# Kernel optimization log

Measured on AMD Instinct MI355X. Metric: run time of the kernel, lower is better.

Reference implementation:

```python
import jax, jax.numpy as jnp
import numpy as np

D = 128        # node_representation_size
V = 100000     # unique_internal_nodes (embedding vocab)
N = 20000      # nodes in the internal graph
E = 640000     # total neighbor (edge) entries


def setup_inputs() -> dict:
    key = jax.random.key(0)
    k1, k2, k3, k4, k5, k6 = jax.random.split(key, 6)
    node_ids = jax.random.randint(k1, (N,), 0, V)
    neighbor_ids = jax.random.randint(k2, (E,), 0, V)
    segment_ids = jnp.sort(jax.random.randint(k3, (E,), 0, N))
    xav = 1.0 / np.sqrt(D)  # xavier_normal std for square [D,D]
    W = jax.random.normal(k4, (D, D), dtype=jnp.float32) * xav
    M = jax.random.normal(k5, (D, D), dtype=jnp.float32) * xav
    emb = jax.random.normal(k6, (V, D), dtype=jnp.float32)
    return {"node_ids": node_ids, "neighbor_ids": neighbor_ids,
            "segment_ids": segment_ids, "W": W, "M": M, "emb": emb}


def reference(node_ids, neighbor_ids, segment_ids, W, M, emb):
    # Per node: s = relu(W @ e[node] + sum_{nbr} M @ e[nbr]); result = sum_nodes s
    self_term = emb[node_ids] @ W.T                       # [N, D]
    nb_msgs = emb[neighbor_ids] @ M.T                     # [E, D]
    nb_agg = jax.ops.segment_sum(nb_msgs, segment_ids, num_segments=N)  # [N, D]
    per_node = jax.nn.relu(self_term + nb_agg)            # [N, D]
    result = per_node.sum(axis=0)                         # [D]
    return jax.nn.softmax(result)[:, None]                # [D, 1], softmax over dim 0
```

## Files before the change

### kernel.cpp

```cpp
#include <hip/hip_runtime.h>

#define D 128
#define RS_STRIDE 64
#define MV_BLOCKS 1024

typedef __attribute__((ext_vector_type(8))) short bf16x8;
typedef __attribute__((ext_vector_type(4))) float f32x4;

__device__ __forceinline__ unsigned short f2bf(float f) {
    unsigned u = __float_as_uint(f);
    unsigned r = (u + 0x7fffu + ((u >> 16) & 1u)) >> 16;
    return (unsigned short)r;
}
__device__ __forceinline__ ushort4 pack4(float4 v) {
    ushort4 o; o.x = f2bf(v.x); o.y = f2bf(v.y); o.z = f2bf(v.z); o.w = f2bf(v.w);
    return o;
}
__device__ __forceinline__ void red3(float& x) {
    x += __shfl_xor(x, 8);
    x += __shfl_xor(x, 16);
    x += __shfl_xor(x, 32);
}

__global__ void rowptr_kernel(const int* __restrict__ seg, int* __restrict__ row_ptr,
                              float* __restrict__ rs, int E, int N) {
    int e = blockIdx.x * blockDim.x + threadIdx.x;
    if (e < D) rs[e * RS_STRIDE] = 0.0f;
    if (e >= E) return;
    int s = seg[e];
    if (e == 0) {
        for (int n = 0; n <= s; ++n) row_ptr[n] = 0;
    } else {
        int sp = seg[e - 1];
        for (int n = sp + 1; n <= s; ++n) row_ptr[n] = e;
    }
    if (e == E - 1) {
        for (int n = s + 1; n <= N; ++n) row_ptr[n] = E;
    }
}

__global__ void prep_kernel(const float* __restrict__ W, const float* __restrict__ M,
                            unsigned short* __restrict__ Wb, unsigned short* __restrict__ Mb) {
    int i = blockIdx.x * blockDim.x + threadIdx.x;
    if (i < D * D) { Wb[i] = f2bf(W[i]); Mb[i] = f2bf(M[i]); }
}

__global__ void agg_kernel(const int* __restrict__ node_ids, const int* __restrict__ nbr,
                           const int* __restrict__ row_ptr, const float* __restrict__ emb,
                           unsigned short* __restrict__ aggb, unsigned short* __restrict__ xb,
                           int N) {
    int n = blockIdx.x * 4 + (threadIdx.x >> 6);
    if (n >= N) return;
    int tt = threadIdx.x & 63;
    int c = tt & 7;
    int j = tt >> 3;

    int lo = row_ptr[n];
    int hi = row_ptr[n + 1];

    float4 s0 = make_float4(0.f, 0.f, 0.f, 0.f);
    float4 s1 = make_float4(0.f, 0.f, 0.f, 0.f);
    float4 s2 = make_float4(0.f, 0.f, 0.f, 0.f);
    float4 s3 = make_float4(0.f, 0.f, 0.f, 0.f);

    for (int e = lo + j; e < hi; e += 8) {
        const float4* r = (const float4*)&emb[(size_t)nbr[e] * D];
        float4 v0 = r[c], v1 = r[c + 8], v2 = r[c + 16], v3 = r[c + 24];
        s0.x += v0.x; s0.y += v0.y; s0.z += v0.z; s0.w += v0.w;
        s1.x += v1.x; s1.y += v1.y; s1.z += v1.z; s1.w += v1.w;
        s2.x += v2.x; s2.y += v2.y; s2.z += v2.z; s2.w += v2.w;
        s3.x += v3.x; s3.y += v3.y; s3.z += v3.z; s3.w += v3.w;
    }
    red3(s0.x); red3(s0.y); red3(s0.z); red3(s0.w);
    red3(s1.x); red3(s1.y); red3(s1.z); red3(s1.w);
    red3(s2.x); red3(s2.y); red3(s2.z); red3(s2.w);
    red3(s3.x); red3(s3.y); red3(s3.z); red3(s3.w);

    if (j == 0) {
        ushort4* o = (ushort4*)(aggb + (size_t)n * D);
        o[c]      = pack4(s0);
        o[c + 8]  = pack4(s1);
        o[c + 16] = pack4(s2);
        o[c + 24] = pack4(s3);
    }
    if (tt < 32) {
        int nid = node_ids[n];
        float4 v = ((const float4*)&emb[(size_t)nid * D])[tt];
        ((ushort4*)(xb + (size_t)n * D))[tt] = pack4(v);
    }
}

__global__ __launch_bounds__(256) void matvec_kernel(
    const unsigned short* __restrict__ xb, const unsigned short* __restrict__ aggb,
    const unsigned short* __restrict__ Wb, const unsigned short* __restrict__ Mb,
    float* __restrict__ rs, int N, int ngroups) {
    int t = threadIdx.x;
    int wid = blockIdx.x * 4 + (t >> 6);
    int l = t & 63;
    int quad = l >> 4, col = l & 15;
    int dt = wid & 7;
    int stripe = wid >> 3;

    bf16x8 bw[4], bm[4];
    int wrow = (dt * 16 + col) * D;
#pragma unroll
    for (int ks = 0; ks < 4; ++ks) {
        int off = wrow + ks * 32 + quad * 8;
        bw[ks] = *(const bf16x8*)(Wb + off);
        bm[ks] = *(const bf16x8*)(Mb + off);
    }

    const bf16x8 zero8 = {0, 0, 0, 0, 0, 0, 0, 0};
    float vsum = 0.f;

    for (int grp = stripe; grp < ngroups; grp += 512) {
        int node = grp * 16 + col;
        bool valid = node < N;
        const unsigned short* xr = xb + (size_t)node * D + quad * 8;
        const unsigned short* ar = aggb + (size_t)node * D + quad * 8;

        f32x4 acc = {0.f, 0.f, 0.f, 0.f};
#pragma unroll
        for (int ks = 0; ks < 4; ++ks) {
            bf16x8 ax = valid ? *(const bf16x8*)(xr + ks * 32) : zero8;
            bf16x8 aa = valid ? *(const bf16x8*)(ar + ks * 32) : zero8;
            acc = __builtin_amdgcn_mfma_f32_16x16x32_bf16(ax, bw[ks], acc, 0, 0, 0);
            acc = __builtin_amdgcn_mfma_f32_16x16x32_bf16(aa, bm[ks], acc, 0, 0, 0);
        }
        vsum += fmaxf(acc[0], 0.f) + fmaxf(acc[1], 0.f)
              + fmaxf(acc[2], 0.f) + fmaxf(acc[3], 0.f);
    }

    vsum += __shfl_xor(vsum, 16);
    vsum += __shfl_xor(vsum, 32);
    if (l < 16) atomicAdd(&rs[(dt * 16 + col) * RS_STRIDE], vsum);
}

__global__ void softmax_kernel(const float* __restrict__ rs, float* __restrict__ out) {
    int t = threadIdx.x;
    float v0 = rs[t * RS_STRIDE];
    float v1 = rs[(t + 64) * RS_STRIDE];
    float m = fmaxf(v0, v1);
    for (int o = 32; o > 0; o >>= 1) m = fmaxf(m, __shfl_xor(m, o));
    float e0 = expf(v0 - m);
    float e1 = expf(v1 - m);
    float s = e0 + e1;
    for (int o = 32; o > 0; o >>= 1) s += __shfl_xor(s, o);
    float inv = 1.0f / s;
    out[t] = e0 * inv;
    out[t + 64] = e1 * inv;
}

extern "C" void kernel_launch(void* const* d_in, const int* in_sizes, int n_in,
                              void* d_out, int out_size, void* d_ws, size_t ws_size,
                              hipStream_t stream) {
    const int*   node_ids = (const int*)d_in[0];
    const int*   nbr      = (const int*)d_in[1];
    const int*   seg      = (const int*)d_in[2];
    const float* W        = (const float*)d_in[3];
    const float* M        = (const float*)d_in[4];
    const float* emb      = (const float*)d_in[5];
    float* out = (float*)d_out;

    int N = in_sizes[0];
    int E = in_sizes[1];
    int ngroups = (N + 15) / 16;

    unsigned short* xb   = (unsigned short*)d_ws;
    unsigned short* aggb = xb + (size_t)N * D;
    unsigned short* Wb   = aggb + (size_t)N * D;
    unsigned short* Mb   = Wb + D * D;
    float* rs            = (float*)(Mb + D * D);
    int* row_ptr         = (int*)(rs + D * RS_STRIDE);

    rowptr_kernel<<<(E + 255) / 256, 256, 0, stream>>>(seg, row_ptr, rs, E, N);
    prep_kernel<<<(D * D + 255) / 256, 256, 0, stream>>>(W, M, Wb, Mb);
    agg_kernel<<<(N + 3) / 4, 256, 0, stream>>>(node_ids, nbr, row_ptr, emb, aggb, xb, N);
    matvec_kernel<<<MV_BLOCKS, 256, 0, stream>>>(xb, aggb, Wb, Mb, rs, N, ngroups);
    softmax_kernel<<<1, 64, 0, stream>>>(rs, out);
}
```

Before: 155.8 us.

## Convert embedding table to bf16 per call and gather bf16 rows

A new conversion kernel turns the whole fp32 embedding table, plus W and M, into bf16 in the workspace on every call. The neighbor aggregation then gathers half-width rows. The self-node gather moves into the MFMA matvec kernel, which reads bf16 rows by node id, so the separate xb buffer goes away. The matvec grid now scales with the group count instead of a fixed block count. In exchange, every call pays a full-table read and write, and neighbor sums are built from bf16-rounded inputs, with an fp32 fallback when the workspace is too small.

```diff
diff --git a/kernel.cpp b/kernel.cpp
--- a/kernel.cpp
+++ b/kernel.cpp
@@ -2,9 +2,9 @@
 
 #define D 128
 #define RS_STRIDE 64
-#define MV_BLOCKS 1024
 
 typedef __attribute__((ext_vector_type(8))) short bf16x8;
+typedef __attribute__((ext_vector_type(8))) unsigned short u16x8;
 typedef __attribute__((ext_vector_type(4))) float f32x4;
 
 __device__ __forceinline__ unsigned short f2bf(float f) {
@@ -12,6 +12,9 @@
     unsigned r = (u + 0x7fffu + ((u >> 16) & 1u)) >> 16;
     return (unsigned short)r;
 }
+__device__ __forceinline__ float bf2f(unsigned short h) {
+    return __uint_as_float(((unsigned)h) << 16);
+}
 __device__ __forceinline__ ushort4 pack4(float4 v) {
     ushort4 o; o.x = f2bf(v.x); o.y = f2bf(v.y); o.z = f2bf(v.z); o.w = f2bf(v.w);
     return o;
@@ -22,10 +25,20 @@
     x += __shfl_xor(x, 32);
 }
 
+__global__ void convert_kernel(const float* __restrict__ emb, const float* __restrict__ W,
+                               const float* __restrict__ M, unsigned short* __restrict__ embb,
+                               unsigned short* __restrict__ Wb, unsigned short* __restrict__ Mb,
+                               float* __restrict__ rs, int n4) {
+    int i = blockIdx.x * blockDim.x + threadIdx.x;
+    if (i < n4) ((ushort4*)embb)[i] = pack4(((const float4*)emb)[i]);
+    if (i < 4096)       ((ushort4*)Wb)[i]        = pack4(((const float4*)W)[i]);
+    else if (i < 8192)  ((ushort4*)Mb)[i - 4096] = pack4(((const float4*)M)[i - 4096]);
+    if (i < D) rs[i * RS_STRIDE] = 0.0f;
+}
+
 __global__ void rowptr_kernel(const int* __restrict__ seg, int* __restrict__ row_ptr,
-                              float* __restrict__ rs, int E, int N) {
+                              int E, int N) {
     int e = blockIdx.x * blockDim.x + threadIdx.x;
-    if (e < D) rs[e * RS_STRIDE] = 0.0f;
     if (e >= E) return;
     int s = seg[e];
     if (e == 0) {
@@ -39,30 +52,56 @@
     }
 }
 
-__global__ void prep_kernel(const float* __restrict__ W, const float* __restrict__ M,
-                            unsigned short* __restrict__ Wb, unsigned short* __restrict__ Mb) {
-    int i = blockIdx.x * blockDim.x + threadIdx.x;
-    if (i < D * D) { Wb[i] = f2bf(W[i]); Mb[i] = f2bf(M[i]); }
-}
-
-__global__ void agg_kernel(const int* __restrict__ node_ids, const int* __restrict__ nbr,
-                           const int* __restrict__ row_ptr, const float* __restrict__ emb,
-                           unsigned short* __restrict__ aggb, unsigned short* __restrict__ xb,
-                           int N) {
+__global__ void agg_bf_kernel(const int* __restrict__ nbr, const int* __restrict__ row_ptr,
+                              const unsigned short* __restrict__ embb,
+                              unsigned short* __restrict__ aggb, int N) {
     int n = blockIdx.x * 4 + (threadIdx.x >> 6);
     if (n >= N) return;
     int tt = threadIdx.x & 63;
     int c = tt & 7;
     int j = tt >> 3;
 
-    int lo = row_ptr[n];
-    int hi = row_ptr[n + 1];
+    int lo = row_ptr[n], hi = row_ptr[n + 1];
+
+    float s0[8], s1[8];
+#pragma unroll
+    for (int k = 0; k < 8; ++k) { s0[k] = 0.f; s1[k] = 0.f; }
+
+    for (int e = lo + j; e < hi; e += 8) {
+        const u16x8* r = (const u16x8*)(embb + (size_t)nbr[e] * D);
+        u16x8 v0 = r[c];
+        u16x8 v1 = r[c + 8];
+#pragma unroll
+        for (int k = 0; k < 8; ++k) { s0[k] += bf2f(v0[k]); s1[k] += bf2f(v1[k]); }
+    }
+#pragma unroll
+    for (int k = 0; k < 8; ++k) { red3(s0[k]); red3(s1[k]); }
+
+    if (j == 0) {
+        u16x8 o0, o1;
+#pragma unroll
+        for (int k = 0; k < 8; ++k) { o0[k] = f2bf(s0[k]); o1[k] = f2bf(s1[k]); }
+        u16x8* o = (u16x8*)(aggb + (size_t)n * D);
+        o[c] = o0;
+        o[c + 8] = o1;
+    }
+}
+
+__global__ void agg_f32_kernel(const int* __restrict__ nbr, const int* __restrict__ row_ptr,
+                               const float* __restrict__ emb,
+                               unsigned short* __restrict__ aggb, int N) {
+    int n = blockIdx.x * 4 + (threadIdx.x >> 6);
+    if (n >= N) return;
+    int tt = threadIdx.x & 63;
+    int c = tt & 7;
+    int j = tt >> 3;
+
+    int lo = row_ptr[n], hi = row_ptr[n + 1];
 
     float4 s0 = make_float4(0.f, 0.f, 0.f, 0.f);
     float4 s1 = make_float4(0.f, 0.f, 0.f, 0.f);
     float4 s2 = make_float4(0.f, 0.f, 0.f, 0.f);
     float4 s3 = make_float4(0.f, 0.f, 0.f, 0.f);
-
     for (int e = lo + j; e < hi; e += 8) {
         const float4* r = (const float4*)&emb[(size_t)nbr[e] * D];
         float4 v0 = r[c], v1 = r[c + 8], v2 = r[c + 16], v3 = r[c + 24];
@@ -75,7 +114,6 @@
     red3(s1.x); red3(s1.y); red3(s1.z); red3(s1.w);
     red3(s2.x); red3(s2.y); red3(s2.z); red3(s2.w);
     red3(s3.x); red3(s3.y); red3(s3.z); red3(s3.w);
-
     if (j == 0) {
         ushort4* o = (ushort4*)(aggb + (size_t)n * D);
         o[c]      = pack4(s0);
@@ -83,17 +121,14 @@
         o[c + 16] = pack4(s2);
         o[c + 24] = pack4(s3);
     }
-    if (tt < 32) {
-        int nid = node_ids[n];
-        float4 v = ((const float4*)&emb[(size_t)nid * D])[tt];
-        ((ushort4*)(xb + (size_t)n * D))[tt] = pack4(v);
-    }
-}
-
+}
+
+template <bool BF>
 __global__ __launch_bounds__(256) void matvec_kernel(
-    const unsigned short* __restrict__ xb, const unsigned short* __restrict__ aggb,
+    const int* __restrict__ node_ids, const void* __restrict__ embv,
+    const unsigned short* __restrict__ aggb,
     const unsigned short* __restrict__ Wb, const unsigned short* __restrict__ Mb,
-    float* __restrict__ rs, int N, int ngroups) {
+    float* __restrict__ rs, int N, int ngroups, int nstripes) {
     int t = threadIdx.x;
     int wid = blockIdx.x * 4 + (t >> 6);
     int l = t & 63;
@@ -113,16 +148,32 @@
     const bf16x8 zero8 = {0, 0, 0, 0, 0, 0, 0, 0};
     float vsum = 0.f;
 
-    for (int grp = stripe; grp < ngroups; grp += 512) {
+    for (int grp = stripe; grp < ngroups; grp += nstripes) {
         int node = grp * 16 + col;
         bool valid = node < N;
-        const unsigned short* xr = xb + (size_t)node * D + quad * 8;
+        int nid = valid ? node_ids[node] : 0;
         const unsigned short* ar = aggb + (size_t)node * D + quad * 8;
 
         f32x4 acc = {0.f, 0.f, 0.f, 0.f};
 #pragma unroll
         for (int ks = 0; ks < 4; ++ks) {
-            bf16x8 ax = valid ? *(const bf16x8*)(xr + ks * 32) : zero8;
+            bf16x8 ax;
+            if (BF) {
+                const unsigned short* xr =
+                    (const unsigned short*)embv + (size_t)nid * D + quad * 8;
+                ax = valid ? *(const bf16x8*)(xr + ks * 32) : zero8;
+            } else {
+                if (valid) {
+                    const float4* xf = (const float4*)((const float*)embv +
+                                       (size_t)nid * D + quad * 8 + ks * 32);
+                    ushort4 p0 = pack4(xf[0]);
+                    ushort4 p1 = pack4(xf[1]);
+                    ax[0] = (short)p0.x; ax[1] = (short)p0.y;
+                    ax[2] = (short)p0.z; ax[3] = (short)p0.w;
+                    ax[4] = (short)p1.x; ax[5] = (short)p1.y;
+                    ax[6] = (short)p1.z; ax[7] = (short)p1.w;
+                } else ax = zero8;
+            }
             bf16x8 aa = valid ? *(const bf16x8*)(ar + ks * 32) : zero8;
             acc = __builtin_amdgcn_mfma_f32_16x16x32_bf16(ax, bw[ks], acc, 0, 0, 0);
             acc = __builtin_amdgcn_mfma_f32_16x16x32_bf16(aa, bm[ks], acc, 0, 0, 0);
@@ -164,18 +215,33 @@
 
     int N = in_sizes[0];
     int E = in_sizes[1];
-    int ngroups = (N + 15) / 16;
-
-    unsigned short* xb   = (unsigned short*)d_ws;
-    unsigned short* aggb = xb + (size_t)N * D;
+    long long VD = in_sizes[5];
+    int ngroups  = (N + 15) / 16;
+    int nstripes = (ngroups + 1) / 2;
+    int mv_blocks = 2 * nstripes;
+
+    unsigned short* aggb = (unsigned short*)d_ws;
     unsigned short* Wb   = aggb + (size_t)N * D;
     unsigned short* Mb   = Wb + D * D;
     float* rs            = (float*)(Mb + D * D);
-    int* row_ptr         = (int*)(rs + D * RS_STRIDE);
-
-    rowptr_kernel<<<(E + 255) / 256, 256, 0, stream>>>(seg, row_ptr, rs, E, N);
-    prep_kernel<<<(D * D + 255) / 256, 256, 0, stream>>>(W, M, Wb, Mb);
-    agg_kernel<<<(N + 3) / 4, 256, 0, stream>>>(node_ids, nbr, row_ptr, emb, aggb, xb, N);
-    matvec_kernel<<<MV_BLOCKS, 256, 0, stream>>>(xb, aggb, Wb, Mb, rs, N, ngroups);
+    int* row_ptr         = (int*)(rs + (size_t)D * RS_STRIDE);
+    unsigned short* embb = (unsigned short*)(row_ptr + (N + 1));
+
+    size_t need_bf = (size_t)(row_ptr + (N + 1) - (int*)d_ws) * 4 + (size_t)VD * 2;
+    bool use_bf = ws_size >= need_bf;
+    int n4 = use_bf ? (int)(VD / 4) : 0;
+    int cvt_n = (n4 > 8192 ? n4 : 8192);
+
+    convert_kernel<<<(cvt_n + 255) / 256, 256, 0, stream>>>(emb, W, M, embb, Wb, Mb, rs, n4);
+    rowptr_kernel<<<(E + 255) / 256, 256, 0, stream>>>(seg, row_ptr, E, N);
+    if (use_bf) {
+        agg_bf_kernel<<<(N + 3) / 4, 256, 0, stream>>>(nbr, row_ptr, embb, aggb, N);
+        matvec_kernel<true><<<mv_blocks, 256, 0, stream>>>(node_ids, embb, aggb, Wb, Mb,
+                                                           rs, N, ngroups, nstripes);
+    } else {
+        agg_f32_kernel<<<(N + 3) / 4, 256, 0, stream>>>(nbr, row_ptr, emb, aggb, N);
+        matvec_kernel<false><<<mv_blocks, 256, 0, stream>>>(node_ids, emb, aggb, Wb, Mb,
+                                                            rs, N, ngroups, nstripes);
+    }
     softmax_kernel<<<1, 64, 0, stream>>>(rs, out);
 }
```

Result: no change. 153.1 us (-1.7%).

## Quantize embedding table to int8 per-row and gather quantized rows in aggregation

Applied to the files above, without the earlier changes.

Adds a prep pass that quantizes the whole embedding table to int8 with a per-row scale. Neighbor aggregation then gathers 128-byte int8 rows instead of 512-byte fp32 rows. The same pass merges row_ptr construction and the W/M bf16 conversion, removing separate launches. The self-term now reads fp32 embedding rows directly inside the matvec kernel instead of staging a bf16 copy, and the matvec grid is resized to the node count. The cost is a full read of the 51 MB table on every call to quantize it, plus int8 rounding error in the neighbor sums.

```diff
diff --git a/kernel.cpp b/kernel.cpp
--- a/kernel.cpp
+++ b/kernel.cpp
@@ -2,9 +2,10 @@
 
 #define D 128
 #define RS_STRIDE 64
-#define MV_BLOCKS 1024
 
 typedef __attribute__((ext_vector_type(8))) short bf16x8;
+typedef __attribute__((ext_vector_type(8))) unsigned short u16x8;
+typedef __attribute__((ext_vector_type(16))) char i8x16;
 typedef __attribute__((ext_vector_type(4))) float f32x4;
 
 __device__ __forceinline__ unsigned short f2bf(float f) {
@@ -16,84 +17,107 @@
     ushort4 o; o.x = f2bf(v.x); o.y = f2bf(v.y); o.z = f2bf(v.z); o.w = f2bf(v.w);
     return o;
 }
-__device__ __forceinline__ void red3(float& x) {
-    x += __shfl_xor(x, 8);
-    x += __shfl_xor(x, 16);
-    x += __shfl_xor(x, 32);
-}
-
-__global__ void rowptr_kernel(const int* __restrict__ seg, int* __restrict__ row_ptr,
-                              float* __restrict__ rs, int E, int N) {
-    int e = blockIdx.x * blockDim.x + threadIdx.x;
-    if (e < D) rs[e * RS_STRIDE] = 0.0f;
-    if (e >= E) return;
-    int s = seg[e];
-    if (e == 0) {
-        for (int n = 0; n <= s; ++n) row_ptr[n] = 0;
-    } else {
-        int sp = seg[e - 1];
-        for (int n = sp + 1; n <= s; ++n) row_ptr[n] = e;
-    }
-    if (e == E - 1) {
-        for (int n = s + 1; n <= N; ++n) row_ptr[n] = E;
-    }
-}
-
-__global__ void prep_kernel(const float* __restrict__ W, const float* __restrict__ M,
-                            unsigned short* __restrict__ Wb, unsigned short* __restrict__ Mb) {
-    int i = blockIdx.x * blockDim.x + threadIdx.x;
-    if (i < D * D) { Wb[i] = f2bf(W[i]); Mb[i] = f2bf(M[i]); }
-}
-
-__global__ void agg_kernel(const int* __restrict__ node_ids, const int* __restrict__ nbr,
-                           const int* __restrict__ row_ptr, const float* __restrict__ emb,
-                           unsigned short* __restrict__ aggb, unsigned short* __restrict__ xb,
-                           int N) {
+
+__global__ void prep_kernel(const float* __restrict__ emb, const float* __restrict__ W,
+                            const float* __restrict__ M, const int* __restrict__ seg,
+                            signed char* __restrict__ q8, float* __restrict__ scale,
+                            unsigned short* __restrict__ Wb, unsigned short* __restrict__ Mb,
+                            float* __restrict__ rs, int* __restrict__ row_ptr,
+                            int V, int E, int N) {
+    int t = threadIdx.x;
+    int gtid = blockIdx.x * 256 + t;
+
+    int r = blockIdx.x * 4 + (t >> 6);
+    if (r < V) {
+        int l = t & 63;
+        float2 v = *(const float2*)(emb + (size_t)r * D + 2 * l);
+        float m = fmaxf(fabsf(v.x), fabsf(v.y));
+        for (int o = 1; o < 64; o <<= 1) m = fmaxf(m, __shfl_xor(m, o));
+        float inv = (m > 0.f) ? 127.0f / m : 0.f;
+        int qa = __float2int_rn(v.x * inv);
+        int qb = __float2int_rn(v.y * inv);
+        qa = min(max(qa, -127), 127);
+        qb = min(max(qb, -127), 127);
+        unsigned short pq = (unsigned short)(((unsigned char)qb << 8) | (unsigned char)qa);
+        *(unsigned short*)(q8 + (size_t)r * D + 2 * l) = pq;
+        if (l == 0) scale[r] = m * (1.0f / 127.0f);
+    }
+
+    if (gtid < 4096)      ((ushort4*)Wb)[gtid]        = pack4(((const float4*)W)[gtid]);
+    else if (gtid < 8192) ((ushort4*)Mb)[gtid - 4096] = pack4(((const float4*)M)[gtid - 4096]);
+    if (gtid < D) rs[gtid * RS_STRIDE] = 0.0f;
+
+    if (gtid < E) {
+        int s = seg[gtid];
+        if (gtid == 0) {
+            for (int n = 0; n <= s; ++n) row_ptr[n] = 0;
+        } else {
+            int sp = seg[gtid - 1];
+            for (int n = sp + 1; n <= s; ++n) row_ptr[n] = gtid;
+        }
+        if (gtid == E - 1) {
+            for (int n = s + 1; n <= N; ++n) row_ptr[n] = E;
+        }
+    }
+}
+
+__global__ void agg_kernel(const int* __restrict__ nbr, const int* __restrict__ row_ptr,
+                           const signed char* __restrict__ q8, const float* __restrict__ scale,
+                           unsigned short* __restrict__ aggb, int N) {
     int n = blockIdx.x * 4 + (threadIdx.x >> 6);
     if (n >= N) return;
     int tt = threadIdx.x & 63;
-    int c = tt & 7;
-    int j = tt >> 3;
-
-    int lo = row_ptr[n];
-    int hi = row_ptr[n + 1];
-
-    float4 s0 = make_float4(0.f, 0.f, 0.f, 0.f);
-    float4 s1 = make_float4(0.f, 0.f, 0.f, 0.f);
-    float4 s2 = make_float4(0.f, 0.f, 0.f, 0.f);
-    float4 s3 = make_float4(0.f, 0.f, 0.f, 0.f);
-
-    for (int e = lo + j; e < hi; e += 8) {
-        const float4* r = (const float4*)&emb[(size_t)nbr[e] * D];
-        float4 v0 = r[c], v1 = r[c + 8], v2 = r[c + 16], v3 = r[c + 24];
-        s0.x += v0.x; s0.y += v0.y; s0.z += v0.z; s0.w += v0.w;
-        s1.x += v1.x; s1.y += v1.y; s1.z += v1.z; s1.w += v1.w;
-        s2.x += v2.x; s2.y += v2.y; s2.z += v2.z; s2.w += v2.w;
-        s3.x += v3.x; s3.y += v3.y; s3.z += v3.z; s3.w += v3.w;
-    }
-    red3(s0.x); red3(s0.y); red3(s0.z); red3(s0.w);
-    red3(s1.x); red3(s1.y); red3(s1.z); red3(s1.w);
-    red3(s2.x); red3(s2.y); red3(s2.z); red3(s2.w);
-    red3(s3.x); red3(s3.y); red3(s3.z); red3(s3.w);
+    int cc = tt & 3;
+    int j  = tt >> 2;
+
+    int lo = row_ptr[n], hi = row_ptr[n + 1];
+
+    float s[32];
+#pragma unroll
+    for (int k = 0; k < 32; ++k) s[k] = 0.f;
+
+    int e = lo + j;
+    int id = (e < hi) ? nbr[e] : -1;
+    while (id >= 0) {
+        const i8x16* r = (const i8x16*)(q8 + (size_t)id * D) + cc * 2;
+        float sc = scale[id];
+        int e2 = e + 16;
+        int id2 = (e2 < hi) ? nbr[e2] : -1;
+        i8x16 p0 = r[0], p1 = r[1];
+#pragma unroll
+        for (int k = 0; k < 16; ++k) {
+            s[k]      = fmaf((float)p0[k], sc, s[k]);
+            s[k + 16] = fmaf((float)p1[k], sc, s[k + 16]);
+        }
+        e = e2; id = id2;
+    }
+#pragma unroll
+    for (int k = 0; k < 32; ++k) {
+        float x = s[k];
+        x += __shfl_xor(x, 4);
+        x += __shfl_xor(x, 8);
+        x += __shfl_xor(x, 16);
+        x += __shfl_xor(x, 32);
+        s[k] = x;
+    }
 
     if (j == 0) {
-        ushort4* o = (ushort4*)(aggb + (size_t)n * D);
-        o[c]      = pack4(s0);
-        o[c + 8]  = pack4(s1);
-        o[c + 16] = pack4(s2);
-        o[c + 24] = pack4(s3);
-    }
-    if (tt < 32) {
-        int nid = node_ids[n];
-        float4 v = ((const float4*)&emb[(size_t)nid * D])[tt];
-        ((ushort4*)(xb + (size_t)n * D))[tt] = pack4(v);
+        u16x8* o = (u16x8*)(aggb + (size_t)n * D) + cc * 4;
+#pragma unroll
+        for (int q = 0; q < 4; ++q) {
+            u16x8 ov;
+#pragma unroll
+            for (int k = 0; k < 8; ++k) ov[k] = f2bf(s[q * 8 + k]);
+            o[q] = ov;
+        }
     }
 }
 
 __global__ __launch_bounds__(256) void matvec_kernel(
-    const unsigned short* __restrict__ xb, const unsigned short* __restrict__ aggb,
+    const int* __restrict__ node_ids, const float* __restrict__ emb,
+    const unsigned short* __restrict__ aggb,
     const unsigned short* __restrict__ Wb, const unsigned short* __restrict__ Mb,
-    float* __restrict__ rs, int N, int ngroups) {
+    float* __restrict__ rs, int N, int ngroups, int nstripes) {
     int t = threadIdx.x;
     int wid = blockIdx.x * 4 + (t >> 6);
     int l = t & 63;
@@ -113,16 +137,25 @@
     const bf16x8 zero8 = {0, 0, 0, 0, 0, 0, 0, 0};
     float vsum = 0.f;
 
-    for (int grp = stripe; grp < ngroups; grp += 512) {
+    for (int grp = stripe; grp < ngroups; grp += nstripes) {
         int node = grp * 16 + col;
         bool valid = node < N;
-        const unsigned short* xr = xb + (size_t)node * D + quad * 8;
+        int nid = valid ? node_ids[node] : 0;
         const unsigned short* ar = aggb + (size_t)node * D + quad * 8;
 
         f32x4 acc = {0.f, 0.f, 0.f, 0.f};
 #pragma unroll
         for (int ks = 0; ks < 4; ++ks) {
-            bf16x8 ax = valid ? *(const bf16x8*)(xr + ks * 32) : zero8;
+            bf16x8 ax;
+            if (valid) {
+                const float4* xf = (const float4*)(emb + (size_t)nid * D + quad * 8 + ks * 32);
+                ushort4 p0 = pack4(xf[0]);
+                ushort4 p1 = pack4(xf[1]);
+                ax[0] = (short)p0.x; ax[1] = (short)p0.y;
+                ax[2] = (short)p0.z; ax[3] = (short)p0.w;
+                ax[4] = (short)p1.x; ax[5] = (short)p1.y;
+                ax[6] = (short)p1.z; ax[7] = (short)p1.w;
+            } else ax = zero8;
             bf16x8 aa = valid ? *(const bf16x8*)(ar + ks * 32) : zero8;
             acc = __builtin_amdgcn_mfma_f32_16x16x32_bf16(ax, bw[ks], acc, 0, 0, 0);
             acc = __builtin_amdgcn_mfma_f32_16x16x32_bf16(aa, bm[ks], acc, 0, 0, 0);
@@ -164,18 +197,29 @@
 
     int N = in_sizes[0];
     int E = in_sizes[1];
-    int ngroups = (N + 15) / 16;
-
-    unsigned short* xb   = (unsigned short*)d_ws;
-    unsigned short* aggb = xb + (size_t)N * D;
-    unsigned short* Wb   = aggb + (size_t)N * D;
+    long long VD = in_sizes[5];
+    int V = (int)(VD / D);
+    int ngroups  = (N + 15) / 16;
+    int nstripes = (ngroups + 1) / 2;
+    int mv_blocks = 2 * nstripes;
+
+    signed char* q8      = (signed char*)d_ws;
+    float* scale         = (float*)(q8 + (size_t)V * D);
+    unsigned short* Wb   = (unsigned short*)(scale + V);
     unsigned short* Mb   = Wb + D * D;
-    float* rs            = (float*)(Mb + D * D);
-    int* row_ptr         = (int*)(rs + D * RS_STRIDE);
-
-    rowptr_kernel<<<(E + 255) / 256, 256, 0, stream>>>(seg, row_ptr, rs, E, N);
-    prep_kernel<<<(D * D + 255) / 256, 256, 0, stream>>>(W, M, Wb, Mb);
-    agg_kernel<<<(N + 3) / 4, 256, 0, stream>>>(node_ids, nbr, row_ptr, emb, aggb, xb, N);
-    matvec_kernel<<<MV_BLOCKS, 256, 0, stream>>>(xb, aggb, Wb, Mb, rs, N, ngroups);
+    unsigned short* aggb = Mb + D * D;
+    float* rs            = (float*)(aggb + (size_t)N * D);
+    int* row_ptr         = (int*)(rs + (size_t)D * RS_STRIDE);
+
+    int prep_blocks = (V + 3) / 4;
+    int min_blocks  = (E + 255) / 256;
+    if (prep_blocks < min_blocks) prep_blocks = min_blocks;
+    if (prep_blocks < 32) prep_blocks = 32;
+
+    prep_kernel<<<prep_blocks, 256, 0, stream>>>(emb, W, M, seg, q8, scale, Wb, Mb,
+                                                 rs, row_ptr, V, E, N);
+    agg_kernel<<<(N + 3) / 4, 256, 0, stream>>>(nbr, row_ptr, q8, scale, aggb, N);
+    matvec_kernel<<<mv_blocks, 256, 0, stream>>>(node_ids, emb, aggb, Wb, Mb,
+                                                 rs, N, ngroups, nstripes);
     softmax_kernel<<<1, 64, 0, stream>>>(rs, out);
 }
```

Result: slower. 159.7 us (+2.5%).
